# Performance work log

Hardware: AMD Instinct MI355X
Metric: run time of the kernel (lower is better)

## Reference

```python
import jax, jax.numpy as jnp
import numpy as np

N_ATOMS = 300000
D_IN = 256


def setup_inputs() -> dict:
    key = jax.random.key(0)
    ks = jax.random.split(key, 8)

    def xavier(k, fan_in, fan_out):
        limit = float(np.sqrt(6.0 / (fan_in + fan_out)))
        return jax.random.uniform(k, (fan_in, fan_out), jnp.float32, -limit, limit)

    density = jax.random.normal(ks[0], (N_ATOMS, D_IN), jnp.float32)
    species = jax.random.randint(ks[1], (N_ATOMS,), -1, 10, jnp.int64)
    return {
        "density": density,
        "species": species,
        "W1": xavier(ks[2], 256, 512), "b1": jnp.zeros((512,), jnp.float32),
        "W2": xavier(ks[3], 512, 512), "b2": jnp.zeros((512,), jnp.float32),
        "W3": xavier(ks[4], 512, 256), "b3": jnp.zeros((256,), jnp.float32),
        "W4": xavier(ks[5], 256, 1),   "b4": jnp.zeros((1,), jnp.float32),
    }


def reference(density, species, W1, b1, W2, b2, W3, b3, W4, b4):
    # Equivalent to torch's nonzero-gather -> MLP -> scatter into zeros:
    # compute the MLP on all rows, then zero rows where species <= -0.5.
    h = jax.nn.silu(density @ W1 + b1)   # [N, 512]
    h = jax.nn.silu(h @ W2 + b2)         # [N, 512]
    h = jax.nn.silu(h @ W3 + b3)         # [N, 256]
    out = h @ W4 + b4                    # [N, 1]
    mask = species > -0.5                # valid atoms
    return jnp.where(mask[:, None], out, jnp.zeros((), out.dtype))
```

## Files before the change

### kernel.cpp

```cpp
#include <hip/hip_runtime.h>

typedef _Float16 half8 __attribute__((ext_vector_type(8)));
typedef _Float16 half4 __attribute__((ext_vector_type(4)));
typedef float f32x4 __attribute__((ext_vector_type(4)));
typedef float f32x16 __attribute__((ext_vector_type(16)));

__global__ void prep_weights(const float* __restrict__ W1, const float* __restrict__ W2,
                             const float* __restrict__ W3, const float* __restrict__ W4,
                             _Float16* __restrict__ wt1, _Float16* __restrict__ wt2,
                             _Float16* __restrict__ wt3, _Float16* __restrict__ w4h) {
  int idx = blockIdx.x * blockDim.x + threadIdx.x;
  if (idx < 512 * 256) {
    int k = idx >> 9, n = idx & 511;
    int off = (((n >> 5) * 16 + (k >> 4)) << 9) + (n & 31) * 8 + (((k >> 3) & 1) << 8) + (k & 7);
    wt1[off] = (_Float16)W1[idx];
    return;
  }
  int i2 = idx - 512 * 256;
  if (i2 < 512 * 512) {
    int k = i2 >> 9, n = i2 & 511;
    int off = (((n >> 5) * 32 + (k >> 4)) << 9) + (n & 31) * 8 + (((k >> 3) & 1) << 8) + (k & 7);
    wt2[off] = (_Float16)W2[i2];
    return;
  }
  int i3 = i2 - 512 * 512;
  if (i3 < 512 * 256) {
    int k = i3 >> 8, n = i3 & 255;
    int off = (((n >> 5) * 32 + (k >> 4)) << 9) + (n & 31) * 8 + (((k >> 3) & 1) << 8) + (k & 7);
    wt3[off] = (_Float16)W3[i3];
    return;
  }
  int i4 = i3 - 512 * 256;
  if (i4 < 256) w4h[i4] = (_Float16)W4[i4];
}

__device__ __forceinline__ float fast_silu(float s) {
  float e = __expf(-s);
  float d = 1.0f + e;
  float r;
  asm("v_rcp_f32 %0, %1" : "=v"(r) : "v"(d));
  return s * r;
}


#define MFMA(a, b, c) __builtin_amdgcn_mfma_f32_32x32x16_f16(a, b, c, 0, 0, 0)

template <int FT, int AT, int KS, int PIN, int POUT>
__device__ __forceinline__ void layer(const _Float16* __restrict__ wt,
                                      const float* __restrict__ bias,
                                      char* __restrict__ Hb,
                                      int wfeat, int lane) {
  const int lr = lane & 31;
  const int lh = lane >> 5;
  const int n0 = wfeat * (FT * 32);
  const int s0 = (lr & 31) << 4;
  const char* Bp = Hb + lr * PIN;
  const char* wp = (const char*)wt + (size_t)(wfeat * FT * KS) * 1024 + lh * 512 + lr * 16;

  f32x16 acc[FT][AT];
#pragma unroll
  for (int f = 0; f < FT; ++f)
#pragma unroll
    for (int rg = 0; rg < 4; ++rg) {
      const int feat = n0 + f * 32 + rg * 8 + lh * 4;
      const f32x4 bv = *(const f32x4*)(bias + feat);
#pragma unroll
      for (int a = 0; a < AT; ++a)
#pragma unroll
        for (int r = 0; r < 4; ++r) acc[f][a][rg * 4 + r] = bv[r];
    }

  half8 Af[FT], Ag[FT], Bf[AT], Bg[AT];
#pragma unroll
  for (int f = 0; f < FT; ++f) Af[f] = *(const half8*)(wp + f * (KS * 1024));
#pragma unroll
  for (int a = 0; a < AT; ++a)
    Bf[a] = *(const half8*)(Bp + a * 32 * PIN + ((lh * 16) ^ s0));

#pragma unroll 1
  for (int ks = 0; ks < KS - 2; ks += 2) {
#pragma unroll
    for (int f = 0; f < FT; ++f)
      Ag[f] = *(const half8*)(wp + f * (KS * 1024) + (ks + 1) * 1024);
#pragma unroll
    for (int a = 0; a < AT; ++a)
      Bg[a] = *(const half8*)(Bp + a * 32 * PIN + (((ks + 1) * 32 + lh * 16) ^ s0));
#pragma unroll
    for (int f = 0; f < FT; ++f)
#pragma unroll
      for (int a = 0; a < AT; ++a) acc[f][a] = MFMA(Af[f], Bf[a], acc[f][a]);
#pragma unroll
    for (int f = 0; f < FT; ++f)
      Af[f] = *(const half8*)(wp + f * (KS * 1024) + (ks + 2) * 1024);
#pragma unroll
    for (int a = 0; a < AT; ++a)
      Bf[a] = *(const half8*)(Bp + a * 32 * PIN + (((ks + 2) * 32 + lh * 16) ^ s0));
#pragma unroll
    for (int f = 0; f < FT; ++f)
#pragma unroll
      for (int a = 0; a < AT; ++a) acc[f][a] = MFMA(Ag[f], Bg[a], acc[f][a]);
  }
#pragma unroll
  for (int f = 0; f < FT; ++f)
    Ag[f] = *(const half8*)(wp + f * (KS * 1024) + (KS - 1) * 1024);
#pragma unroll
  for (int a = 0; a < AT; ++a)
    Bg[a] = *(const half8*)(Bp + a * 32 * PIN + ((((KS - 1) * 32) + lh * 16) ^ s0));
#pragma unroll
  for (int f = 0; f < FT; ++f)
#pragma unroll
    for (int a = 0; a < AT; ++a) acc[f][a] = MFMA(Af[f], Bf[a], acc[f][a]);
#pragma unroll
  for (int f = 0; f < FT; ++f)
#pragma unroll
    for (int a = 0; a < AT; ++a) acc[f][a] = MFMA(Ag[f], Bg[a], acc[f][a]);

#pragma unroll
  for (int f = 0; f < FT; ++f)
#pragma unroll
    for (int a = 0; a < AT; ++a)
#pragma unroll
      for (int j = 0; j < 16; ++j) acc[f][a][j] = fast_silu(acc[f][a][j]);

  __syncthreads();

#pragma unroll
  for (int f = 0; f < FT; ++f) {
#pragma unroll
    for (int rg = 0; rg < 4; ++rg) {
      const int feat = n0 + f * 32 + rg * 8 + lh * 4;
#pragma unroll
      for (int a = 0; a < AT; ++a) {
        half4 h;
#pragma unroll
        for (int r = 0; r < 4; ++r) h[r] = (_Float16)acc[f][a][rg * 4 + r];
        const int row = a * 32 + lr;
        *(half4*)(Hb + row * POUT + ((feat * 2) ^ ((row & 31) << 4))) = h;
      }
    }
  }
}

extern "C" __global__ void __launch_bounds__(512, 4)
mlp_kernel(const float* __restrict__ X, const int* __restrict__ species,
           const _Float16* __restrict__ wt1, const float* __restrict__ b1,
           const _Float16* __restrict__ wt2, const float* __restrict__ b2,
           const _Float16* __restrict__ wt3, const float* __restrict__ b3,
           const _Float16* __restrict__ w4h, const float* __restrict__ b4,
           float* __restrict__ out, int natoms) {
  __shared__ __align__(16) char H[64 * 1024];
  const int tid = threadIdx.x;
  const int lane = tid & 63;
  const int wid = tid >> 6;
  const long abase = (long)blockIdx.x * 64;

  {
    const int r = tid >> 3, cg = tid & 7;
    long g = abase + r;
    const long gmax = (long)natoms - 1;
    if (g > gmax) g = gmax;
    const float* xp = X + g * 256;
    const int sw = (r & 31) << 4;
#pragma unroll
    for (int j = 0; j < 8; ++j) {
      const int colh = cg * 4 + j * 32;
      f32x4 v = *(const f32x4*)(xp + colh);
      half4 h;
#pragma unroll
      for (int e = 0; e < 4; ++e) h[e] = (_Float16)v[e];
      *(half4*)(H + r * 512 + ((colh * 2) ^ sw)) = h;
    }
  }
  __syncthreads();

  layer<2, 2, 16, 512, 1024>(wt1, b1, H, wid, lane);
  __syncthreads();
  layer<2, 2, 32, 1024, 1024>(wt2, b2, H, wid, lane);
  __syncthreads();
  layer<1, 2, 32, 1024, 1024>(wt3, b3, H, wid, lane);
  __syncthreads();

  const int atom = tid >> 3, part = tid & 7;
  const int sw = (atom & 31) << 4;
  const char* h3 = H + atom * 1024;
  const _Float16* w4p = w4h + part * 32;
  float sum = 0.0f;
#pragma unroll
  for (int j = 0; j < 4; ++j) {
    half8 h = *(const half8*)(h3 + ((part * 64 + j * 16) ^ sw));
    half8 w = *(const half8*)(w4p + j * 8);
#pragma unroll
    for (int e = 0; e < 8; ++e) sum += (float)h[e] * (float)w[e];
  }
  sum += __shfl_xor(sum, 1);
  sum += __shfl_xor(sum, 2);
  sum += __shfl_xor(sum, 4);
  if (part == 0) {
    const long g = abase + atom;
    if (g < natoms) {
      float r = sum + b4[0];
      out[g] = (species[g] >= 0) ? r : 0.0f;
    }
  }
}

extern "C" void kernel_launch(void* const* d_in, const int* in_sizes, int n_in,
                              void* d_out, int out_size, void* d_ws, size_t ws_size,
                              hipStream_t stream) {
  const float* X = (const float*)d_in[0];
  const int* species = (const int*)d_in[1];
  const float* W1 = (const float*)d_in[2];
  const float* b1 = (const float*)d_in[3];
  const float* W2 = (const float*)d_in[4];
  const float* b2 = (const float*)d_in[5];
  const float* W3 = (const float*)d_in[6];
  const float* b3 = (const float*)d_in[7];
  const float* W4 = (const float*)d_in[8];
  const float* b4 = (const float*)d_in[9];
  float* out = (float*)d_out;
  const int natoms = in_sizes[0] / 256;

  char* ws = (char*)d_ws;
  _Float16* wt1 = (_Float16*)(ws);
  _Float16* wt2 = (_Float16*)(ws + 262144);
  _Float16* wt3 = (_Float16*)(ws + 262144 + 524288);
  _Float16* w4h = (_Float16*)(ws + 262144 + 524288 + 262144);

  const int prep_total = 512 * 256 + 512 * 512 + 256 * 512 + 256;
  hipLaunchKernelGGL(prep_weights, dim3((prep_total + 255) / 256), dim3(256), 0, stream,
                     W1, W2, W3, W4, wt1, wt2, wt3, w4h);

  const int nblocks = (natoms + 63) / 64;
  hipLaunchKernelGGL(mlp_kernel, dim3(nblocks), dim3(512), 0, stream,
                     X, species, wt1, b1, wt2, b2, wt3, b3, w4h, b4, out, natoms);
}
```

Baseline: 395.8 us.

## Compact valid atoms before MLP to skip masked rows

Adds a compaction kernel that uses wave ballots and an atomic counter to gather indices of atoms with species >= 0, and writes zeros directly for masked atoms. The MLP kernel then processes only the compacted atoms, gathering input rows by index and scattering results, with blocks beyond the valid count exiting early. This removes the roughly 9% of GEMM work spent on masked atoms, at the cost of an extra memset and launch, indirect gathers of the input, and a dependence on workspace size.

```diff
diff --git a/kernel.cpp b/kernel.cpp
--- a/kernel.cpp
+++ b/kernel.cpp
@@ -32,6 +32,26 @@
   }
   int i4 = i3 - 512 * 256;
   if (i4 < 256) w4h[i4] = (_Float16)W4[i4];
+}
+
+extern "C" __global__ void compact_kernel(const int* __restrict__ species,
+                                          int* __restrict__ idx,
+                                          int* __restrict__ count,
+                                          float* __restrict__ out, int natoms) {
+  int i = blockIdx.x * blockDim.x + threadIdx.x;
+  if (i >= natoms) return;
+  bool valid = species[i] >= 0;
+  unsigned long long m = __ballot(valid);
+  int lane = threadIdx.x & 63;
+  int base = 0;
+  if (lane == 0 && m) base = atomicAdd(count, (int)__popcll(m));
+  base = __shfl(base, 0);
+  if (valid) {
+    int off = (int)__popcll(m & ((1ull << lane) - 1));
+    idx[base + off] = i;
+  } else {
+    out[i] = 0.0f;
+  }
 }
 
 __device__ __forceinline__ float fast_silu(float s) {
@@ -147,18 +167,26 @@
            const _Float16* __restrict__ wt2, const float* __restrict__ b2,
            const _Float16* __restrict__ wt3, const float* __restrict__ b3,
            const _Float16* __restrict__ w4h, const float* __restrict__ b4,
-           float* __restrict__ out, int natoms) {
+           float* __restrict__ out, int natoms,
+           const int* __restrict__ idx, const int* __restrict__ dcount) {
   __shared__ __align__(16) char H[64 * 1024];
   const int tid = threadIdx.x;
   const int lane = tid & 63;
   const int wid = tid >> 6;
   const long abase = (long)blockIdx.x * 64;
 
+  int nvalid = natoms;
+  if (idx) {
+    nvalid = *dcount;
+    if (abase >= nvalid) return;
+  }
+
   {
     const int r = tid >> 3, cg = tid & 7;
-    long g = abase + r;
-    const long gmax = (long)natoms - 1;
-    if (g > gmax) g = gmax;
+    long li = abase + r;
+    const long lmax = (long)nvalid - 1;
+    if (li > lmax) li = lmax;
+    const long g = idx ? (long)idx[li] : li;
     const float* xp = X + g * 256;
     const int sw = (r & 31) << 4;
 #pragma unroll
@@ -196,10 +224,14 @@
   sum += __shfl_xor(sum, 2);
   sum += __shfl_xor(sum, 4);
   if (part == 0) {
-    const long g = abase + atom;
-    if (g < natoms) {
+    const long li = abase + atom;
+    if (li < nvalid) {
       float r = sum + b4[0];
-      out[g] = (species[g] >= 0) ? r : 0.0f;
+      if (idx) {
+        out[idx[li]] = r;
+      } else {
+        out[li] = (species[li] >= 0) ? r : 0.0f;
+      }
     }
   }
 }
@@ -225,12 +257,25 @@
   _Float16* wt2 = (_Float16*)(ws + 262144);
   _Float16* wt3 = (_Float16*)(ws + 262144 + 524288);
   _Float16* w4h = (_Float16*)(ws + 262144 + 524288 + 262144);
+  int* dcount = (int*)(ws + 1049088);
+  int* didx = (int*)(ws + 1052672);
+
+  const size_t ws_needed = 1052672 + (size_t)natoms * 4;
+  const bool use_compact = (ws_size >= ws_needed);
 
   const int prep_total = 512 * 256 + 512 * 512 + 256 * 512 + 256;
   hipLaunchKernelGGL(prep_weights, dim3((prep_total + 255) / 256), dim3(256), 0, stream,
                      W1, W2, W3, W4, wt1, wt2, wt3, w4h);
 
+  if (use_compact) {
+    hipMemsetAsync(dcount, 0, 4, stream);
+    hipLaunchKernelGGL(compact_kernel, dim3((natoms + 255) / 256), dim3(256), 0, stream,
+                       species, didx, dcount, out, natoms);
+  }
+
   const int nblocks = (natoms + 63) / 64;
   hipLaunchKernelGGL(mlp_kernel, dim3(nblocks), dim3(512), 0, stream,
-                     X, species, wt1, b1, wt2, b2, wt3, b3, w4h, b4, out, natoms);
-}
+                     X, species, wt1, b1, wt2, b2, wt3, b3, w4h, b4, out, natoms,
+                     use_compact ? didx : (const int*)nullptr,
+                     use_compact ? (const int*)dcount : (const int*)nullptr);
+}
```

New measurement: 404.7 us. 2.2% more time.

## Compact valid atoms and run MLP only on species-valid rows

Applied to the files above, without the earlier changes.

Adds a stream-compaction pass, fused into the weight-prep kernel, that writes per-chunk counts and indices of atoms with species >= 0, and zeroes the output for masked atoms. The MLP kernel then scans the chunk counts into a shared-memory prefix, maps each compacted row to its original atom through a binary search, and exits blocks that fall past the valid count. This avoids doing the MLP on the roughly 9% of atoms that are masked out. In exchange every block pays for a 2048-entry prefix scan, gathered row loads and scattered output writes, and the kernel uses more shared memory.

```diff
diff --git a/kernel.cpp b/kernel.cpp
--- a/kernel.cpp
+++ b/kernel.cpp
@@ -5,10 +5,37 @@
 typedef float f32x4 __attribute__((ext_vector_type(4)));
 typedef float f32x16 __attribute__((ext_vector_type(16)));
 
-__global__ void prep_weights(const float* __restrict__ W1, const float* __restrict__ W2,
+#define NCHUNK_MAX 2048
+
+__global__ void prep_compact(const float* __restrict__ W1, const float* __restrict__ W2,
                              const float* __restrict__ W3, const float* __restrict__ W4,
                              _Float16* __restrict__ wt1, _Float16* __restrict__ wt2,
-                             _Float16* __restrict__ wt3, _Float16* __restrict__ w4h) {
+                             _Float16* __restrict__ wt3, _Float16* __restrict__ w4h,
+                             const int* __restrict__ species, int* __restrict__ idxloc,
+                             int* __restrict__ cnt, float* __restrict__ out,
+                             int natoms, int nprep) {
+  __shared__ int wsum[4];
+  if (blockIdx.x >= nprep) {
+    const int c = blockIdx.x - nprep;
+    const int i = c * 256 + threadIdx.x;
+    const bool valid = (i < natoms) && (species[i] >= 0);
+    const unsigned long long m = __ballot(valid);
+    const int lane = threadIdx.x & 63, w = threadIdx.x >> 6;
+    if (lane == 0) wsum[w] = (int)__popcll(m);
+    __syncthreads();
+    int base = 0;
+#pragma unroll
+    for (int k = 0; k < 4; ++k)
+      if (k < w) base += wsum[k];
+    if (valid) {
+      int off = (int)__popcll(m & ((1ull << lane) - 1));
+      idxloc[c * 256 + base + off] = i;
+    } else if (i < natoms) {
+      out[i] = 0.0f;
+    }
+    if (threadIdx.x == 0) cnt[c] = wsum[0] + wsum[1] + wsum[2] + wsum[3];
+    return;
+  }
   int idx = blockIdx.x * blockDim.x + threadIdx.x;
   if (idx < 512 * 256) {
     int k = idx >> 9, n = idx & 511;
@@ -147,18 +174,69 @@
            const _Float16* __restrict__ wt2, const float* __restrict__ b2,
            const _Float16* __restrict__ wt3, const float* __restrict__ b3,
            const _Float16* __restrict__ w4h, const float* __restrict__ b4,
-           float* __restrict__ out, int natoms) {
+           float* __restrict__ out, int natoms,
+           const int* __restrict__ idxloc, const int* __restrict__ cnt, int nchunks) {
   __shared__ __align__(16) char H[64 * 1024];
+  __shared__ int prefixS[NCHUNK_MAX + 1];
+  __shared__ int gidx[64];
+  __shared__ int wtot[8];
   const int tid = threadIdx.x;
   const int lane = tid & 63;
   const int wid = tid >> 6;
   const long abase = (long)blockIdx.x * 64;
 
+  int nvalid = natoms;
+  if (idxloc) {
+    int v[4];
+    int tsum = 0;
+#pragma unroll
+    for (int j = 0; j < 4; ++j) {
+      const int c = tid * 4 + j;
+      v[j] = (c < nchunks) ? cnt[c] : 0;
+      tsum += v[j];
+    }
+    int ws_ = tsum;
+#pragma unroll
+    for (int d = 1; d < 64; d <<= 1) {
+      int o = __shfl_up(ws_, d);
+      if (lane >= d) ws_ += o;
+    }
+    if (lane == 63) wtot[wid] = ws_;
+    __syncthreads();
+    int wbase = 0, tot = 0;
+#pragma unroll
+    for (int k = 0; k < 8; ++k) {
+      if (k < wid) wbase += wtot[k];
+      tot += wtot[k];
+    }
+    int run = wbase + ws_ - tsum;
+#pragma unroll
+    for (int j = 0; j < 4; ++j) {
+      const int c = tid * 4 + j;
+      if (c < nchunks) prefixS[c] = run;
+      run += v[j];
+    }
+    if (tid == 0) prefixS[nchunks] = tot;
+    nvalid = tot;
+    __syncthreads();
+    if (abase >= nvalid) return;
+  }
+
   {
     const int r = tid >> 3, cg = tid & 7;
-    long g = abase + r;
-    const long gmax = (long)natoms - 1;
-    if (g > gmax) g = gmax;
+    long li = abase + r;
+    const long lmax = (long)nvalid - 1;
+    if (li > lmax) li = lmax;
+    long g = li;
+    if (idxloc) {
+      int lo = 0, hi = nchunks - 1;
+      while (lo < hi) {
+        int mid = (lo + hi + 1) >> 1;
+        if (prefixS[mid] <= (int)li) lo = mid; else hi = mid - 1;
+      }
+      g = idxloc[lo * 256 + ((int)li - prefixS[lo])];
+      if (cg == 0) gidx[r] = (int)g;
+    }
     const float* xp = X + g * 256;
     const int sw = (r & 31) << 4;
 #pragma unroll
@@ -196,10 +274,14 @@
   sum += __shfl_xor(sum, 2);
   sum += __shfl_xor(sum, 4);
   if (part == 0) {
-    const long g = abase + atom;
-    if (g < natoms) {
+    const long li = abase + atom;
+    if (li < nvalid) {
       float r = sum + b4[0];
-      out[g] = (species[g] >= 0) ? r : 0.0f;
+      if (idxloc) {
+        out[gidx[atom]] = r;
+      } else {
+        out[li] = (species[li] >= 0) ? r : 0.0f;
+      }
     }
   }
 }
@@ -225,12 +307,23 @@
   _Float16* wt2 = (_Float16*)(ws + 262144);
   _Float16* wt3 = (_Float16*)(ws + 262144 + 524288);
   _Float16* w4h = (_Float16*)(ws + 262144 + 524288 + 262144);
+  int* cnt = (int*)(ws + 1049088);
+  int* idxloc = (int*)(ws + 1049088 + 8192);
+
+  const int nchunks = (natoms + 255) / 256;
+  const size_t ws_needed = 1049088 + 8192 + (size_t)natoms * 4;
+  const bool use_compact = (ws_size >= ws_needed) && (nchunks <= NCHUNK_MAX);
 
   const int prep_total = 512 * 256 + 512 * 512 + 256 * 512 + 256;
-  hipLaunchKernelGGL(prep_weights, dim3((prep_total + 255) / 256), dim3(256), 0, stream,
-                     W1, W2, W3, W4, wt1, wt2, wt3, w4h);
+  const int nprep = (prep_total + 255) / 256;
+  const int nblk = nprep + (use_compact ? nchunks : 0);
+  hipLaunchKernelGGL(prep_compact, dim3(nblk), dim3(256), 0, stream,
+                     W1, W2, W3, W4, wt1, wt2, wt3, w4h,
+                     species, idxloc, cnt, out, natoms, nprep);
 
   const int nblocks = (natoms + 63) / 64;
   hipLaunchKernelGGL(mlp_kernel, dim3(nblocks), dim3(512), 0, stream,
-                     X, species, wt1, b1, wt2, b2, wt3, b3, w4h, b4, out, natoms);
-}
+                     X, species, wt1, b1, wt2, b2, wt3, b3, w4h, b4, out, natoms,
+                     use_compact ? idxloc : (const int*)nullptr,
+                     use_compact ? (const int*)cnt : (const int*)nullptr, nchunks);
+}
```

Measured after the change: 360.4 us. 1.1x faster.
